# Kernel tuning notes

Hardware: AMD Instinct MI355X
Metric: run time of the kernel (lower is better)

The kernel has to match this reference:

```python
import jax, jax.numpy as jnp
import numpy as np

# ---- static config (mirrors LSSTransform defaults) ----
B, N, CIN, CT = 4, 6, 512, 64
OGH, OGW, DS = 256, 704, 16
FH, FW = OGH // DS, OGW // DS            # 16, 44
DB0, DB1, DBS = 4.0, 45.0, 1.0
D = int((DB1 - DB0) / DBS)               # 41 depth bins
NXX, NYY, NZZ = 128, 128, 1              # BEV grid from x/y/z bounds
DXv = np.array([0.8, 0.8, 20.0], np.float32)            # dx
BXv = np.array([-51.2 + 0.4, -51.2 + 0.4, 0.0], np.float32)  # bx = lower + dx/2


def _frustum():
    # (D, fH, fW, 3) of (pixel_u, pixel_v, depth), as in create_frustum
    ds = np.broadcast_to(np.arange(DB0, DB1, DBS, dtype=np.float32)[:, None, None], (D, FH, FW))
    xs = np.broadcast_to(np.linspace(0, OGW - 1, FW, dtype=np.float32)[None, None, :], (D, FH, FW))
    ys = np.broadcast_to(np.linspace(0, OGH - 1, FH, dtype=np.float32)[None, :, None], (D, FH, FW))
    return jnp.asarray(np.stack([xs, ys, ds], axis=-1))

FRUSTUM = _frustum()


def setup_inputs() -> dict:
    key = jax.random.key(0)
    k0, k1, k2 = jax.random.split(key, 3)
    x = jax.random.normal(k0, (B, N, CIN, FH, FW), jnp.float32)
    # camera->ego rotation: ego = (z_cam, x_cam, y_cam), so depth maps to ego-x
    R = jnp.array([[0., 0., 1.], [1., 0., 0.], [0., 1., 0.]], jnp.float32)
    rots = jnp.broadcast_to(R, (B, N, 3, 3)) + 0.0
    trans = 0.5 * jax.random.normal(k1, (B, N, 3), jnp.float32)
    K = jnp.array([[500., 0., OGW / 2.], [0., 500., OGH / 2.], [0., 0., 1.]], jnp.float32)
    intrins = jnp.broadcast_to(K, (B, N, 3, 3)) + 0.0
    post_rots = jnp.broadcast_to(jnp.eye(3, dtype=jnp.float32), (B, N, 3, 3)) + 0.0
    post_trans = jnp.zeros((B, N, 3), jnp.float32)
    Wd = 0.02 * jax.random.normal(k2, (D + CT, CIN), jnp.float32)  # depthnet 1x1 conv weight
    bd = jnp.zeros((D + CT,), jnp.float32)
    return dict(x=x, rots=rots, trans=trans, intrins=intrins,
                post_rots=post_rots, post_trans=post_trans, Wd=Wd, bd=bd)


def _forward(x, rots, trans, intrins, post_rots, post_trans, Wd, bd):
    # depthnet: 1x1 conv == channel matmul
    feat = jnp.einsum('bnchw,oc->bnohw', x, Wd) + bd[None, None, :, None, None]
    depth = jax.nn.softmax(feat[:, :, :D], axis=2)          # (B,N,D,H,W)
    cvt = feat[:, :, D:D + CT]                              # (B,N,CT,H,W)
    vol = depth[:, :, None] * cvt[:, :, :, None]            # (B,N,CT,D,H,W)
    vol = jnp.transpose(vol, (0, 1, 3, 4, 5, 2))            # (B,N,D,H,W,CT)

    # get_geometry: undo image augs, unproject, cam->ego
    pts = FRUSTUM[None, None] - post_trans[:, :, None, None, None, :]
    pts = jnp.einsum('bnij,bndhwj->bndhwi', jnp.linalg.inv(post_rots), pts)
    pts = jnp.concatenate([pts[..., :2] * pts[..., 2:3], pts[..., 2:3]], axis=-1)
    comb = rots @ jnp.linalg.inv(intrins)
    pts = jnp.einsum('bnij,bndhwj->bndhwi', comb, pts) + trans[:, :, None, None, None, :]

    # voxel_pooling: truncating cast matches torch .long()
    g = ((pts - (jnp.asarray(BXv) - jnp.asarray(DXv) / 2.0)) / jnp.asarray(DXv)).astype(jnp.int32)
    gx, gy, gz = g[..., 0], g[..., 1], g[..., 2]
    kept = (gx >= 0) & (gx < NXX) & (gy >= 0) & (gy < NYY) & (gz >= 0) & (gz < NZZ)
    bix = jnp.arange(B, dtype=jnp.int32)[:, None, None, None, None]
    vox = ((bix * NZZ + gz) * NYY + gy) * NXX + gx          # flat voxel id per point
    TOT = B * NZZ * NYY * NXX
    seg = jnp.where(kept, vox, TOT).reshape(-1)             # invalid -> trash bucket
    feats = vol.reshape(-1, CT)                             # (Nprime, CT)
    sums = jax.ops.segment_sum(feats, seg, num_segments=TOT + 1)[:TOT]
    final = sums.reshape(B, NZZ, NYY, NXX, CT)
    # (B, C, nz, ny, nx) then cat over z into channels -> (B, nz*C, ny, nx)
    final = jnp.transpose(final, (0, 1, 4, 2, 3)).reshape(B, NZZ * CT, NYY, NXX)
    return final


def reference(x, rots, trans, intrins, post_rots, post_trans, Wd, bd):
    return _forward(x, rots, trans, intrins, post_rots, post_trans, Wd, bd)
```

## Files before the change

kernel.cpp:

```cpp
#include <hip/hip_runtime.h>
#include <hip/hip_bf16.h>
#include <math.h>

#define B_   4
#define N_   6
#define CIN  512
#define CT   64
#define Dd   41
#define FH   16
#define FW   44
#define NPIX 704
#define NO   105
#define DSTR 48
#define NXX  128
#define NYY  128
#define NZZ  1
#define TOT  (B_*NZZ*NYY*NXX)
#define NPTS (B_*N_*Dd*NPIX)
#define NCHUNK ((NPTS+63)/64)

#define WSTRIDE 520

#define GEMM_BLOCKS 1056
#define GEOM_BLOCKS 4224

typedef __attribute__((ext_vector_type(8))) short short8;
typedef __attribute__((ext_vector_type(4))) float f32x4;


__device__ __forceinline__ unsigned short f2bf(float f) {
    unsigned u = __float_as_uint(f);
    u += 0x7FFFu + ((u >> 16) & 1u);
    return (unsigned short)(u >> 16);
}

__device__ __forceinline__ void inv3(const double* m, double* o) {
    double a=m[0],b=m[1],c=m[2],d=m[3],e=m[4],f=m[5],g=m[6],h=m[7],i=m[8];
    double A  =  (e*i - f*h);
    double Bc = -(d*i - f*g);
    double Cc =  (d*h - e*g);
    double det = a*A + b*Bc + c*Cc;
    double inv = 1.0/det;
    o[0]=A*inv;            o[1]=-(b*i - c*h)*inv;  o[2]= (b*f - c*e)*inv;
    o[3]=Bc*inv;           o[4]= (a*i - c*g)*inv;  o[5]=-(a*f - c*d)*inv;
    o[6]=Cc*inv;           o[7]=-(a*h - b*g)*inv;  o[8]= (a*e - b*d)*inv;
}

__device__ __forceinline__ void geom_lane(const double* s_tf, int b, int pix, int l,
                                          bool& kept, int& vox) {
    const int hh = pix / FW, ww = pix % FW;
    const double fx = (double)((float)(ww * (703.0/43.0)));
    const double fy = (double)((float)(hh * 17.0));
    const double px = fx - s_tf[21], py = fy - s_tf[22], mz = -s_tf[23];
    const double qx0 = s_tf[ 9]*px + s_tf[10]*py + s_tf[11]*mz, qx1 = s_tf[11];
    const double qy0 = s_tf[12]*px + s_tf[13]*py + s_tf[14]*mz, qy1 = s_tf[14];
    const double qz0 = s_tf[15]*px + s_tf[16]*py + s_tf[17]*mz, qz1 = s_tf[17];
    const double ux0 = s_tf[0]*qx0 + s_tf[1]*qy0 + s_tf[2], ux1 = s_tf[0]*qx1 + s_tf[1]*qy1;
    const double uy0 = s_tf[3]*qx0 + s_tf[4]*qy0 + s_tf[5], uy1 = s_tf[3]*qx1 + s_tf[4]*qy1;
    const double uz0 = s_tf[6]*qx0 + s_tf[7]*qy0 + s_tf[8], uz1 = s_tf[6]*qx1 + s_tf[7]*qy1;
    const double t0 = s_tf[18], t1 = s_tf[19], t2 = s_tf[20];

    const double DXD = (double)0.8f;
    const double LOX = (double)(-50.8f) - DXD*0.5;
    const double LOY = LOX;
    const double DZD = 20.0;
    const double LOZ = -10.0;

    kept = false; vox = 0;
    if (l < Dd) {
        double fz = 4.0 + (double)l;
        double qz = qz0 + qz1*fz;
        double sx = qz*(ux0 + ux1*fz) + t0;
        double sy = qz*(uy0 + uy1*fz) + t1;
        double sz = qz*(uz0 + uz1*fz) + t2;
        int gx = (int)((sx - LOX) / DXD);
        int gy = (int)((sy - LOY) / DXD);
        int gz = (int)((sz - LOZ) / DZD);
        kept = (gx>=0) & (gx<NXX) & (gy>=0) & (gy<NYY) & (gz>=0) & (gz<NZZ);
        vox  = (((b*NZZ + gz)*NYY + gy)*NXX + gx);
    }
}

__global__ __launch_bounds__(256) void prep_kernel(
    const float* __restrict__ rots, const float* __restrict__ trans,
    const float* __restrict__ intrins, const float* __restrict__ post_rots,
    const float* __restrict__ post_trans, const float* __restrict__ Wd,
    const float* __restrict__ x,
    double* __restrict__ tf, unsigned short* __restrict__ WdB,
    unsigned short* __restrict__ xB)
{
    const int t = threadIdx.x;
    if (blockIdx.x < 2112) {
        __shared__ float s_x[64*65];
        const int p    = blockIdx.x;
        const int bn   = p / 88;
        const int r    = p % 88;
        const int kg   = r / 11;
        const int tile = r % 11;
        const int pix0 = tile * 64;

        const float* src = x + ((size_t)bn*CIN + kg*64)*NPIX + pix0;
        #pragma unroll
        for (int i = 0; i < 16; i++) {
            int idx = i*256 + t;
            int k  = idx >> 6;
            int px = idx & 63;
            s_x[k*65 + px] = src[(size_t)k*NPIX + px];
        }
        __syncthreads();

        const int px  = t & 63;
        #pragma unroll
        for (int pass = 0; pass < 2; pass++) {
            int k8l = (t >> 6) + 4*pass;
            unsigned pk[4];
            #pragma unroll
            for (int i = 0; i < 4; i++) {
                float a = s_x[(k8l*8 + 2*i    )*65 + px];
                float c = s_x[(k8l*8 + 2*i + 1)*65 + px];
                pk[i] = (unsigned)f2bf(a) | ((unsigned)f2bf(c) << 16);
            }
            unsigned* dst = (unsigned*)&xB[(((size_t)(bn*64 + kg*8 + k8l))*NPIX + pix0 + px)*8];
            *(uint4*)dst = make_uint4(pk[0], pk[1], pk[2], pk[3]);
        }
    } else {
        int b2 = blockIdx.x - 2112;
        int idx = b2*256 + t;
        if (idx < 128*CIN) {
            int o = idx / CIN;
            WdB[idx] = (o < NO) ? f2bf(Wd[idx]) : (unsigned short)0;
        }
        if (b2 == 0 && t < B_*N_) {
            int bn = t;
            double k[9], pr[9], r[9], ik[9], ipr[9], c[9];
            for (int i=0;i<9;i++) { k[i]=intrins[bn*9+i]; pr[i]=post_rots[bn*9+i]; r[i]=rots[bn*9+i]; }
            inv3(k, ik);
            inv3(pr, ipr);
            for (int i=0;i<3;i++)
                for (int j=0;j<3;j++) {
                    double s = 0.0;
                    for (int kk=0;kk<3;kk++) s += r[i*3+kk]*ik[kk*3+j];
                    c[i*3+j] = s;
                }
            double* o = tf + bn*24;
            for (int i=0;i<9;i++) o[i]   = c[i];
            for (int i=0;i<9;i++) o[9+i] = ipr[i];
            for (int i=0;i<3;i++) o[18+i] = (double)trans[bn*3+i];
            for (int i=0;i<3;i++) o[21+i] = (double)post_trans[bn*3+i];
        }
    }
}

__global__ __launch_bounds__(256) void gemm_geom_kernel(
    const unsigned short* __restrict__ xB, const unsigned short* __restrict__ WdB,
    const float* __restrict__ bd, const double* __restrict__ tf,
    float* __restrict__ featD, float* __restrict__ featB,
    int* __restrict__ hist, int* __restrict__ rank_arr)
{
    __shared__ unsigned short s_wd[32*WSTRIDE];
    __shared__ double s_tf[24];

    const int t    = threadIdx.x;
    const int l    = t & 63;
    const int wv   = t >> 6;

    if (blockIdx.x < GEMM_BLOCKS) {
        const int col  = l & 15;
        const int quad = l >> 4;
        const int xcd = blockIdx.x & 7;
        const int q   = blockIdx.x >> 3;
        const int s   = q & 3;
        const int pg  = q >> 2;
        const int p   = pg*8 + xcd;
        const int bn   = p / 11;
        const int tile = p % 11;
        const int pix0 = tile * 64;

        {
            const int o  = t >> 3;
            const int c8 = t & 7;
            const unsigned short* srcw = WdB + (size_t)(s*32 + o)*CIN;
            #pragma unroll
            for (int i = 0; i < 8; i++) {
                int k = c8*8 + i*64;
                *(uint4*)&s_wd[o*WSTRIDE + k] = *(const uint4*)&srcw[k];
            }
        }
        __syncthreads();

        f32x4 acc[2];
        acc[0] = (f32x4){0.f,0.f,0.f,0.f};
        acc[1] = (f32x4){0.f,0.f,0.f,0.f};

        const int pix = pix0 + wv*16 + col;
        const unsigned short* xbase = xB + (((size_t)(bn*64))*NPIX)*8;

        #pragma unroll
        for (int ks = 0; ks < 16; ks++) {
            const int k8 = ks*4 + quad;
            short8 bfr = *(const short8*)&xbase[((size_t)k8*NPIX + pix)*8];
            #pragma unroll
            for (int j = 0; j < 2; j++) {
                short8 afr = *(const short8*)&s_wd[(j*16 + col)*WSTRIDE + ks*32 + quad*8];
                acc[j] = __builtin_amdgcn_mfma_f32_16x16x32_bf16(afr, bfr, acc[j], 0, 0, 0);
            }
        }

        const size_t prow = (size_t)(bn*NPIX + pix);
        #pragma unroll
        for (int j = 0; j < 2; j++) {
            #pragma unroll
            for (int rr = 0; rr < 4; rr++) {
                int o = (2*s + j)*16 + quad*4 + rr;
                if (o < Dd) {
                    featD[prow*DSTR + o] = acc[j][rr] + bd[o];
                } else if (o < NO) {
                    featB[prow*CT + (o - Dd)] = acc[j][rr] + bd[o];
                }
            }
        }
    } else {
        const int bid2 = blockIdx.x - GEMM_BLOCKS;
        const int bid  = (bid2 & 7) * 528 + (bid2 >> 3);
        const int bn  = bid / 176;
        const int pix = (bid % 176)*4 + wv;
        const int b   = bn / N_;

        if (t < 24) s_tf[t] = tf[bn*24 + t];
        __syncthreads();

        bool kept; int vox;
        geom_lane(s_tf, b, pix, l, kept, vox);
        if (kept) {
            int rank = atomicAdd(&hist[vox], 1);
            rank_arr[(size_t)(bn*NPIX + pix)*Dd + l] = rank;
        }
    }
}

__global__ __launch_bounds__(256) void scan1_kernel(const int* __restrict__ hist,
                                                    int* __restrict__ offs,
                                                    int* __restrict__ bsum) {
    __shared__ int s[256];
    const int t = threadIdx.x;
    const int i = blockIdx.x*256 + t;
    int val = hist[i];
    s[t] = val;
    __syncthreads();
    #pragma unroll
    for (int off = 1; off < 256; off <<= 1) {
        int u = (t >= off) ? s[t-off] : 0;
        __syncthreads();
        s[t] += u;
        __syncthreads();
    }
    offs[i] = s[t] - val;
    if (t == 255) bsum[blockIdx.x] = s[255];
}

__global__ __launch_bounds__(256) void scan2_kernel(int* __restrict__ bsum,
                                                    int* __restrict__ np) {
    __shared__ int s[256];
    const int t = threadIdx.x;
    int v = bsum[t];
    s[t] = v;
    __syncthreads();
    #pragma unroll
    for (int off = 1; off < 256; off <<= 1) {
        int u = (t >= off) ? s[t-off] : 0;
        __syncthreads();
        s[t] += u;
        __syncthreads();
    }
    bsum[t] = s[t] - v;
    if (t == 255) np[0] = s[255];
}

__global__ __launch_bounds__(256) void sm_scatter_kernel(
    const float* __restrict__ featD, const double* __restrict__ tf,
    const int* __restrict__ offs, const int* __restrict__ bsum,
    const int* __restrict__ rank_arr, uint2* __restrict__ rec)
{
    __shared__ double s_tf[24];
    const int bid = (blockIdx.x & 7) * 528 + (blockIdx.x >> 3);
    const int t   = threadIdx.x;
    const int l   = t & 63;
    const int wv  = t >> 6;
    const int bn  = bid / 176;
    const int pix = (bid % 176)*4 + wv;
    const int b   = bn / N_;

    if (t < 24) s_tf[t] = tf[bn*24 + t];
    __syncthreads();

    const size_t prow = (size_t)(bn*NPIX + pix);

    float logit = (l < Dd) ? featD[prow*DSTR + l] : -3.0e38f;
    float mm = logit;
    #pragma unroll
    for (int off = 32; off > 0; off >>= 1) mm = fmaxf(mm, __shfl_xor(mm, off));
    float e = (l < Dd) ? expf(logit - mm) : 0.0f;
    float ssum = e;
    #pragma unroll
    for (int off = 32; off > 0; off >>= 1) ssum += __shfl_xor(ssum, off);
    const float wgt = e / ssum;

    bool kept; int vox;
    geom_lane(s_tf, b, pix, l, kept, vox);
    if (kept) {
        int pos = offs[vox] + bsum[vox >> 8] + rank_arr[prow*Dd + l];
        unsigned pk = ((unsigned)vox << 15) | (unsigned)prow;
        rec[pos] = make_uint2(pk, __float_as_uint(wgt));
    }
}

__global__ __launch_bounds__(256) void gather_kernel(
    const uint2* __restrict__ rec, const int* __restrict__ np,
    const float* __restrict__ featB, float* __restrict__ scat)
{
    const int bid = (blockIdx.x & 7) * 339 + (blockIdx.x >> 3);
    const int t  = threadIdx.x;
    const int wv = t >> 6;
    const int l  = t & 63;
    const int chunk = bid * 4 + wv;
    const int base  = chunk * 64;
    const int Np = np[0];
    if (base >= Np) return;
    int cnt = Np - base; if (cnt > 64) cnt = 64;

    unsigned pk = 0; float w = 0.0f;
    if (l < cnt) { uint2 r = rec[base + l]; pk = r.x; w = __uint_as_float(r.y); }
    unsigned pkm = __shfl(pk, (l == 0) ? 0 : (l - 1));
    unsigned long long starts =
        __ballot((l > 0) && (l < cnt) && ((pk >> 15) != (pkm >> 15)));

    unsigned long long m = starts;
    int rs = 0;
    while (rs < cnt) {
        int re = m ? (__ffsll((unsigned long long)m) - 1) : cnt;
        if (m) m &= m - 1;
        float acc = 0.0f;
        for (int j = rs; j < re; j++) {
            unsigned pkj = __shfl(pk, j);
            float    wj  = __shfl(w, j);
            unsigned id  = pkj & 0x7FFFu;
            acc += wj * featB[(size_t)id * CT + l];
        }
        unsigned vrun = __shfl(pk, rs) >> 15;
        float* dst = scat + (size_t)vrun * CT + l;
        if (rs == 0 || re == cnt) {
            unsafeAtomicAdd(dst, acc);
        } else {
            *dst = acc;
        }
        rs = re;
    }
}

__global__ __launch_bounds__(256) void transpose_k(const float* __restrict__ scat,
                                                   float* __restrict__ out) {
    __shared__ float tile[64][65];
    int b  = blockIdx.x >> 8;
    int t0 = (blockIdx.x & 255) * 64;
    const float* src = scat + (size_t)b * (NYY*NXX) * CT;
    #pragma unroll
    for (int i=0;i<16;i++) {
        int idx = threadIdx.x + i*256;
        int p = idx >> 6, c = idx & 63;
        tile[p][c] = src[(size_t)(t0+p)*CT + c];
    }
    __syncthreads();
    float* dst = out + (size_t)b * CT * (NYY*NXX);
    #pragma unroll
    for (int i=0;i<16;i++) {
        int idx = threadIdx.x + i*256;
        int c = idx >> 6, p = idx & 63;
        dst[(size_t)c*(NYY*NXX) + t0 + p] = tile[p][c];
    }
}

extern "C" void kernel_launch(void* const* d_in, const int* in_sizes, int n_in,
                              void* d_out, int out_size, void* d_ws, size_t ws_size,
                              hipStream_t stream) {
    const float* x          = (const float*)d_in[0];
    const float* rots       = (const float*)d_in[1];
    const float* trans      = (const float*)d_in[2];
    const float* intrins    = (const float*)d_in[3];
    const float* post_rots  = (const float*)d_in[4];
    const float* post_trans = (const float*)d_in[5];
    const float* Wd         = (const float*)d_in[6];
    const float* bd         = (const float*)d_in[7];
    float* out = (float*)d_out;

    char* ws = (char*)d_ws;
    float*          featB  = (float*)ws;          ws += (size_t)B_*N_*NPIX*CT*4;
    float*          featD  = (float*)ws;          ws += (size_t)B_*N_*NPIX*DSTR*4;
    char*           Xreg   = ws;                  ws += (size_t)B_*N_*CIN*NPIX*2;
    int*            rank_a = (int*)ws;            ws += (size_t)NPTS*4;
    uint2*          rec    = (uint2*)ws;          ws += (size_t)NPTS*8;
    int*            hist   = (int*)ws;            ws += (size_t)TOT*4;
    int*            offs   = (int*)ws;            ws += (size_t)TOT*4;
    int*            bsum   = (int*)ws;            ws += 256*4;
    int*            np     = (int*)ws;            ws += 256;
    double*         tf     = (double*)ws;         ws += (size_t)B_*N_*24*8;
    unsigned short* WdB    = (unsigned short*)ws; ws += (size_t)128*CIN*2;

    unsigned short* xB   = (unsigned short*)Xreg;
    float*          scat = (float*)Xreg;

    hipMemsetAsync(hist, 0, (size_t)TOT*4, stream);
    prep_kernel<<<2368, 256, 0, stream>>>(rots, trans, intrins, post_rots, post_trans,
                                          Wd, x, tf, WdB, xB);
    gemm_geom_kernel<<<GEMM_BLOCKS + GEOM_BLOCKS, 256, 0, stream>>>(
        xB, WdB, bd, tf, featD, featB, hist, rank_a);
    hipMemsetAsync(scat, 0, (size_t)TOT*CT*4, stream);
    scan1_kernel<<<TOT/256, 256, 0, stream>>>(hist, offs, bsum);
    scan2_kernel<<<1, 256, 0, stream>>>(bsum, np);
    sm_scatter_kernel<<<B_*N_*176, 256, 0, stream>>>(featD, tf, offs, bsum, rank_a, rec);
    gather_kernel<<<2712, 256, 0, stream>>>(rec, np, featB, scat);
    transpose_k<<<B_*(NYY*NXX/64), 256, 0, stream>>>(scat, out);
}
```

Measured before the change: 208.9 us.

## Fold memsets into kernels, vectorize x staging, halve GEMM weight LDS

Removes the two hipMemsetAsync calls: the hist zeroing moves into extra blocks of prep_kernel, and the scatter buffer zeroing moves into scan1_kernel with float4 stores. The prep transpose now loads x with float4 into an LDS tile padded to stride 68. The GEMM stages the weights in two 16-row halves, halving LDS use to allow more occupancy at the cost of extra barriers. The scan loop's barriers are also rearranged. These changes aim to cut launch count and memory-transfer overhead.

```diff
diff --git a/kernel.cpp b/kernel.cpp
--- a/kernel.cpp
+++ b/kernel.cpp
@@ -87,11 +87,11 @@
     const float* __restrict__ post_trans, const float* __restrict__ Wd,
     const float* __restrict__ x,
     double* __restrict__ tf, unsigned short* __restrict__ WdB,
-    unsigned short* __restrict__ xB)
+    unsigned short* __restrict__ xB, int* __restrict__ hist)
 {
     const int t = threadIdx.x;
     if (blockIdx.x < 2112) {
-        __shared__ float s_x[64*65];
+        __shared__ float s_x[64*68];
         const int p    = blockIdx.x;
         const int bn   = p / 88;
         const int r    = p % 88;
@@ -101,11 +101,12 @@
 
         const float* src = x + ((size_t)bn*CIN + kg*64)*NPIX + pix0;
         #pragma unroll
-        for (int i = 0; i < 16; i++) {
+        for (int i = 0; i < 4; i++) {
             int idx = i*256 + t;
-            int k  = idx >> 6;
-            int px = idx & 63;
-            s_x[k*65 + px] = src[(size_t)k*NPIX + px];
+            int k   = idx >> 4;
+            int px4 = (idx & 15) * 4;
+            float4 v = *(const float4*)&src[(size_t)k*NPIX + px4];
+            *(float4*)&s_x[k*68 + px4] = v;
         }
         __syncthreads();
 
@@ -116,14 +117,14 @@
             unsigned pk[4];
             #pragma unroll
             for (int i = 0; i < 4; i++) {
-                float a = s_x[(k8l*8 + 2*i    )*65 + px];
-                float c = s_x[(k8l*8 + 2*i + 1)*65 + px];
+                float a = s_x[(k8l*8 + 2*i    )*68 + px];
+                float c = s_x[(k8l*8 + 2*i + 1)*68 + px];
                 pk[i] = (unsigned)f2bf(a) | ((unsigned)f2bf(c) << 16);
             }
             unsigned* dst = (unsigned*)&xB[(((size_t)(bn*64 + kg*8 + k8l))*NPIX + pix0 + px)*8];
             *(uint4*)dst = make_uint4(pk[0], pk[1], pk[2], pk[3]);
         }
-    } else {
+    } else if (blockIdx.x < 2368) {
         int b2 = blockIdx.x - 2112;
         int idx = b2*256 + t;
         if (idx < 128*CIN) {
@@ -148,6 +149,9 @@
             for (int i=0;i<3;i++) o[18+i] = (double)trans[bn*3+i];
             for (int i=0;i<3;i++) o[21+i] = (double)post_trans[bn*3+i];
         }
+    } else {
+        int b3 = blockIdx.x - 2368;
+        hist[b3*256 + t] = 0;
     }
 }
 
@@ -157,7 +161,7 @@
     float* __restrict__ featD, float* __restrict__ featB,
     int* __restrict__ hist, int* __restrict__ rank_arr)
 {
-    __shared__ unsigned short s_wd[32*WSTRIDE];
+    __shared__ unsigned short s_wd[16*WSTRIDE];
     __shared__ double s_tf[24];
 
     const int t    = threadIdx.x;
@@ -176,34 +180,39 @@
         const int tile = p % 11;
         const int pix0 = tile * 64;
 
-        {
-            const int o  = t >> 3;
-            const int c8 = t & 7;
-            const unsigned short* srcw = WdB + (size_t)(s*32 + o)*CIN;
-            #pragma unroll
-            for (int i = 0; i < 8; i++) {
-                int k = c8*8 + i*64;
-                *(uint4*)&s_wd[o*WSTRIDE + k] = *(const uint4*)&srcw[k];
-            }
-        }
-        __syncthreads();
+        const int pix = pix0 + wv*16 + col;
+        const unsigned short* xbase = xB + (((size_t)(bn*64))*NPIX)*8;
 
         f32x4 acc[2];
         acc[0] = (f32x4){0.f,0.f,0.f,0.f};
         acc[1] = (f32x4){0.f,0.f,0.f,0.f};
 
-        const int pix = pix0 + wv*16 + col;
-        const unsigned short* xbase = xB + (((size_t)(bn*64))*NPIX)*8;
-
         #pragma unroll
-        for (int ks = 0; ks < 16; ks++) {
-            const int k8 = ks*4 + quad;
-            short8 bfr = *(const short8*)&xbase[((size_t)k8*NPIX + pix)*8];
+        for (int half = 0; half < 2; half++) {
+            {
+                const int o  = t >> 4;
+                const int c  = t & 15;
+                const unsigned short* srcw = WdB + (size_t)(s*32 + half*16 + o)*CIN + c*32;
+                uint4 v0 = *(const uint4*)(srcw + 0);
+                uint4 v1 = *(const uint4*)(srcw + 8);
+                uint4 v2 = *(const uint4*)(srcw + 16);
+                uint4 v3 = *(const uint4*)(srcw + 24);
+                unsigned short* dstw = &s_wd[o*WSTRIDE + c*32];
+                *(uint4*)(dstw + 0)  = v0;
+                *(uint4*)(dstw + 8)  = v1;
+                *(uint4*)(dstw + 16) = v2;
+                *(uint4*)(dstw + 24) = v3;
+            }
+            __syncthreads();
+
             #pragma unroll
-            for (int j = 0; j < 2; j++) {
-                short8 afr = *(const short8*)&s_wd[(j*16 + col)*WSTRIDE + ks*32 + quad*8];
-                acc[j] = __builtin_amdgcn_mfma_f32_16x16x32_bf16(afr, bfr, acc[j], 0, 0, 0);
+            for (int ks = 0; ks < 16; ks++) {
+                const int k8 = ks*4 + quad;
+                short8 bfr = *(const short8*)&xbase[((size_t)k8*NPIX + pix)*8];
+                short8 afr = *(const short8*)&s_wd[col*WSTRIDE + ks*32 + quad*8];
+                acc[half] = __builtin_amdgcn_mfma_f32_16x16x32_bf16(afr, bfr, acc[half], 0, 0, 0);
             }
+            __syncthreads();
         }
 
         const size_t prow = (size_t)(bn*NPIX + pix);
@@ -240,20 +249,30 @@
 
 __global__ __launch_bounds__(256) void scan1_kernel(const int* __restrict__ hist,
                                                     int* __restrict__ offs,
-                                                    int* __restrict__ bsum) {
+                                                    int* __restrict__ bsum,
+                                                    float4* __restrict__ scat4) {
     __shared__ int s[256];
     const int t = threadIdx.x;
     const int i = blockIdx.x*256 + t;
     int val = hist[i];
     s[t] = val;
     __syncthreads();
+
+    {
+        float4 z = make_float4(0.f, 0.f, 0.f, 0.f);
+        float4* dst = scat4 + (size_t)blockIdx.x*4096 + t;
+        #pragma unroll
+        for (int j = 0; j < 16; j++) dst[j*256] = z;
+    }
+
     #pragma unroll
     for (int off = 1; off < 256; off <<= 1) {
+        __syncthreads();
         int u = (t >= off) ? s[t-off] : 0;
         __syncthreads();
         s[t] += u;
-        __syncthreads();
-    }
+    }
+    __syncthreads();
     offs[i] = s[t] - val;
     if (t == 255) bsum[blockIdx.x] = s[255];
 }
@@ -408,13 +427,11 @@
     unsigned short* xB   = (unsigned short*)Xreg;
     float*          scat = (float*)Xreg;
 
-    hipMemsetAsync(hist, 0, (size_t)TOT*4, stream);
-    prep_kernel<<<2368, 256, 0, stream>>>(rots, trans, intrins, post_rots, post_trans,
-                                          Wd, x, tf, WdB, xB);
+    prep_kernel<<<2624, 256, 0, stream>>>(rots, trans, intrins, post_rots, post_trans,
+                                          Wd, x, tf, WdB, xB, hist);
     gemm_geom_kernel<<<GEMM_BLOCKS + GEOM_BLOCKS, 256, 0, stream>>>(
         xB, WdB, bd, tf, featD, featB, hist, rank_a);
-    hipMemsetAsync(scat, 0, (size_t)TOT*CT*4, stream);
-    scan1_kernel<<<TOT/256, 256, 0, stream>>>(hist, offs, bsum);
+    scan1_kernel<<<TOT/256, 256, 0, stream>>>(hist, offs, bsum, (float4*)scat);
     scan2_kernel<<<1, 256, 0, stream>>>(bsum, np);
     sm_scatter_kernel<<<B_*N_*176, 256, 0, stream>>>(featD, tf, offs, bsum, rank_a, rec);
     gather_kernel<<<2712, 256, 0, stream>>>(rec, np, featB, scat);
```

Measured after the change: 206.1 us. Within noise of the previous version (-1.4%).
